# Optimization experiments

Hardware: AMD Instinct MI355X
Metric: run time of the kernel (lower is better)

Reference implementation:

```python
import jax, jax.numpy as jnp
import numpy as np

N, E, F, R, L, B = 50000, 800000, 64, 20, 2, 64
RC = 5.0
ZMAX = 100
LN2 = 0.6931471805599453

def ssp(x):
    # shifted softplus: softplus(x) - log(2)
    return jax.nn.softplus(x) - LN2

def setup_inputs() -> dict:
    key = jax.random.key(0)
    ks = jax.random.split(key, 32)
    w = lambda i, shape: jax.random.normal(ks[i], shape, dtype=jnp.float32) * 0.05
    inp = {
        'z': jax.random.randint(ks[0], (N,), 0, ZMAX + 1),
        'pos': jax.random.normal(ks[1], (N, 3), dtype=jnp.float32) * 3.0,
        'edge_index': jax.random.randint(ks[2], (2, E), 0, N),
        'batch_idx': jnp.sort(jax.random.randint(ks[3], (N,), 0, B)),
        'emb': jax.random.normal(ks[4], (ZMAX + 1, F), dtype=jnp.float32),
        'phi_W': w(5, (L, 3 * F, F)), 'phi_b': w(6, (L, 3 * F)),
        'filt_W1': w(7, (L, F, R)), 'filt_b1': w(8, (L, F)),
        'filt_W2': w(9, (L, 3 * F, F)), 'filt_b2': w(10, (L, 3 * F)),
        'U_W': w(11, (L, F, F)), 'V_W': w(12, (L, F, F)),
        'a_W1': w(13, (L, F, 2 * F)), 'a_b1': w(14, (L, F)),
        'a_W2': w(15, (L, 3 * F, F)), 'a_b2': w(16, (L, 3 * F)),
        'e_W1': w(17, (F // 2, F)), 'e_b1': w(18, (F // 2,)),
        'e_W2': w(19, (1, F // 2)), 'e_b2': w(20, (1,)),
        'dip_w': w(21, (F,)),
    }
    return inp

def reference(z, pos, edge_index, batch_idx, emb, phi_W, phi_b,
              filt_W1, filt_b1, filt_W2, filt_b2, U_W, V_W,
              a_W1, a_b1, a_W2, a_b2, e_W1, e_b1, e_W2, e_b2, dip_w):
    src, dst = edge_index[0], edge_index[1]
    s = emb[z]                               # (N, F)
    v = jnp.zeros((N, F, 3), dtype=s.dtype)  # (N, F, 3)

    # edge geometry
    r_vec = pos[dst] - pos[src]              # (E, 3)
    r_norm = jnp.linalg.norm(r_vec, axis=-1)
    r_hat = r_vec / jnp.maximum(r_norm, 1e-8)[:, None]
    # Gaussian RBF on [0, RC], widths = grid spacing
    mu = jnp.linspace(0.0, RC, R, dtype=s.dtype)
    width = mu[1] - mu[0]
    e_ij = jnp.exp(-((r_norm[:, None] - mu[None, :]) ** 2) / (2.0 * width * width))
    fc = 0.5 * (jnp.cos(jnp.pi * r_norm / RC) + 1.0) * (r_norm < RC)
    e_ij = e_ij * fc[:, None]                # (E, R)

    for l in range(L):
        # message block
        filt = ssp(e_ij @ filt_W1[l].T + filt_b1[l]) @ filt_W2[l].T + filt_b2[l]  # (E, 3F)
        W_s, W_v, W_r = jnp.split(filt, 3, axis=-1)
        phi = s[dst] @ phi_W[l].T + phi_b[l]                                       # (E, 3F)
        phi_s, phi_v, phi_r = jnp.split(phi, 3, axis=-1)
        m_s = W_s * phi_s                                                          # (E, F)
        m_v = W_v[:, :, None] * v[dst] + (W_r * phi_r)[:, :, None] * r_hat[:, None, :]  # (E, F, 3)
        s = s + jax.ops.segment_sum(m_s, src, num_segments=N)
        v = v + jax.ops.segment_sum(m_v, src, num_segments=N)
        # update block
        Uv = jnp.einsum('nfd,gf->ngd', v, U_W[l])
        Vv = jnp.einsum('nfd,gf->ngd', v, V_W[l])
        Vv_norm_sq = jnp.sum(Vv * Vv, axis=-1)                                     # (N, F)
        a = ssp(jnp.concatenate([s, Vv_norm_sq], axis=-1) @ a_W1[l].T + a_b1[l]) @ a_W2[l].T + a_b2[l]
        a_ss, a_sv, a_vv = jnp.split(a, 3, axis=-1)
        inner = jnp.sum(Uv * Vv, axis=-1)
        s = s + a_ss + a_sv * inner
        v = v + a_vv[:, :, None] * Uv

    # heads
    eps_i = (ssp(s @ e_W1.T + e_b1) @ e_W2.T + e_b2)[:, 0]  # (N,)
    energy = jax.ops.segment_sum(eps_i, batch_idx, num_segments=B)
    mu_i = jnp.sum(v * dip_w[None, :, None], axis=1)         # (N, 3)
    mu_mol = jax.ops.segment_sum(mu_i, batch_idx, num_segments=B)
    dipole = jnp.linalg.norm(mu_mol, axis=-1)
    charges = jnp.zeros((N,), dtype=s.dtype)
    return energy, dipole, charges
```

## Files before the change

### kernel.cpp

```cpp
#include <hip/hip_runtime.h>
#include <math.h>

static constexpr int N  = 50000;
static constexpr int E  = 800000;
static constexpr int F  = 64;
static constexpr int R  = 20;
static constexpr int NL = 2;
static constexpr int B  = 64;
static constexpr float RC   = 5.0f;
static constexpr float LN2F = 0.6931471805599453f;
static constexpr float WIDTH  = RC / (R - 1);
static constexpr float INV2W2 = 1.0f / (2.0f * WIDTH * WIDTH);
static constexpr float PI_F = 3.14159265358979323846f;

static constexpr int   NB     = 4096;
static constexpr float DR     = RC / NB;
static constexpr float INV_DR = NB / RC;
static constexpr int   IZERO  = NB + 1;
static constexpr int   TENTA  = NB + 2;

static constexpr int NBLK_SCAN = (N + 255) / 256;

typedef __attribute__((ext_vector_type(8))) short bf16x8;
typedef __attribute__((ext_vector_type(4))) float f32x4;
typedef __attribute__((ext_vector_type(3))) unsigned uint32x3;

__device__ __forceinline__ float ssp_f(float x) {
    return fmaxf(x, 0.0f) + log1pf(__expf(-fabsf(x))) - LN2F;
}

__device__ __forceinline__ short f2bf(float x) {
    unsigned u = __builtin_bit_cast(unsigned, x);
    unsigned r = (u + 0x7fffu + ((u >> 16) & 1u)) >> 16;
    return (short)r;
}
__device__ __forceinline__ float bf_lo(unsigned u) {
    return __builtin_bit_cast(float, u << 16);
}
__device__ __forceinline__ float bf_hi(unsigned u) {
    return __builtin_bit_cast(float, u & 0xffff0000u);
}

__global__ void k_hist(const int* __restrict__ ei, int* __restrict__ cnt) {
    int e = blockIdx.x * blockDim.x + threadIdx.x;
    if (e < E) atomicAdd(&cnt[ei[e]], 1);
}

__global__ void k_scan_a(const int* __restrict__ cnt, int* __restrict__ bsum) {
    __shared__ int part[256];
    const int t = threadIdx.x;
    const int idx = blockIdx.x * 256 + t;
    int v = (idx < N) ? ((cnt[idx] + 1) & ~1) : 0;
    part[t] = v;
    __syncthreads();
    for (int d = 1; d < 256; d <<= 1) {
        int x = (t >= d) ? part[t - d] : 0;
        __syncthreads();
        part[t] += x;
        __syncthreads();
    }
    if (t == 255) bsum[blockIdx.x] = part[255];
}

__global__ void k_scan_b(const int* __restrict__ bsum, int* __restrict__ bpre,
                         int* __restrict__ offN) {
    __shared__ int part[256];
    const int t = threadIdx.x;
    int v = (t < NBLK_SCAN) ? bsum[t] : 0;
    part[t] = v;
    __syncthreads();
    for (int d = 1; d < 256; d <<= 1) {
        int x = (t >= d) ? part[t - d] : 0;
        __syncthreads();
        part[t] += x;
        __syncthreads();
    }
    if (t < NBLK_SCAN) bpre[t] = part[t] - v;
    if (t == NBLK_SCAN - 1) *offN = part[t];
}

__global__ void k_scan_c(const int* __restrict__ cnt, const int* __restrict__ bpre,
                         int* __restrict__ off, int* __restrict__ cur,
                         uint4* __restrict__ edata) {
    __shared__ int part[256];
    const int t = threadIdx.x;
    const int idx = blockIdx.x * 256 + t;
    int vraw = (idx < N) ? cnt[idx] : 0;
    int v = (vraw + 1) & ~1;
    part[t] = v;
    __syncthreads();
    for (int d = 1; d < 256; d <<= 1) {
        int x = (t >= d) ? part[t - d] : 0;
        __syncthreads();
        part[t] += x;
        __syncthreads();
    }
    if (idx < N) {
        int e = bpre[blockIdx.x] + part[t] - v;
        off[idx] = e;
        cur[idx] = e;
        if (vraw & 1) {
            uint4 nil;
            nil.x = (unsigned)idx * 256u;
            nil.y = (unsigned)IZERO * 512u;
            nil.z = 0u; nil.w = 0u;
            edata[e + vraw] = nil;
        }
    }
}

__global__ void k_scatter(const int* __restrict__ ei, int* __restrict__ cur,
                          const float* __restrict__ pos, uint4* __restrict__ edata) {
    int e = blockIdx.x * blockDim.x + threadIdx.x;
    if (e >= E) return;
    int src = ei[e], dst = ei[E + e];
    int p = atomicAdd(&cur[src], 1);
    float qx = pos[dst * 3 + 0] - pos[src * 3 + 0];
    float qy = pos[dst * 3 + 1] - pos[src * 3 + 1];
    float qz = pos[dst * 3 + 2] - pos[src * 3 + 2];
    float rn = sqrtf(qx * qx + qy * qy + qz * qz);
    float invn = 1.0f / fmaxf(rn, 1e-8f);
    int i = (int)(rn * INV_DR + 0.5f);
    if (i > NB) i = NB;
    uint4 rec;
    rec.x = (unsigned)dst * 256u;
    rec.y = (unsigned)i * 512u;
    rec.z = (unsigned)(unsigned short)f2bf(qx * invn)
          | ((unsigned)(unsigned short)f2bf(qy * invn) << 16);
    rec.w = (unsigned)(unsigned short)f2bf(qz * invn);
    edata[p] = rec;
}

__global__ void k_table(const float* __restrict__ fW1, const float* __restrict__ fb1,
                        const float* __restrict__ fW2, const float* __restrict__ fb2,
                        unsigned short* __restrict__ Tp) {
    __shared__ float sh[4][F];
    const int wid  = threadIdx.x >> 6;
    const int lane = threadIdx.x & 63;
    const int gid  = blockIdx.x * 4 + wid;
    if (gid >= NL * (NB + 1)) return;
    const int l   = gid / (NB + 1);
    const int row = gid % (NB + 1);
    const float r = (float)row * DR;
    const float fc = (r < RC) ? 0.5f * (__cosf(PI_F * r * (1.0f / RC)) + 1.0f) : 0.0f;

    float acc = fb1[l * F + lane];
    const float* w1 = fW1 + (size_t)l * F * R + (size_t)lane * R;
    #pragma unroll
    for (int rr = 0; rr < R; rr++) {
        float dmu = r - rr * WIDTH;
        float er = __expf(-dmu * dmu * INV2W2) * fc;
        acc = fmaf(er, w1[rr], acc);
    }
    sh[wid][lane] = ssp_f(acc);
    __syncthreads();
    unsigned short* TpL = Tp + (size_t)l * TENTA * 256;
    #pragma unroll
    for (int p = 0; p < 3; p++) {
        int c = p * 64 + lane;
        float a = fb2[l * 192 + c];
        const float* w2 = fW2 + ((size_t)l * 192 + c) * 64;
        #pragma unroll 8
        for (int k = 0; k < F; k++) a = fmaf(sh[wid][k], w2[k], a);
        TpL[(size_t)row * 256 + lane * 4 + p] = (unsigned short)f2bf(a);
    }
    TpL[(size_t)row * 256 + lane * 4 + 3] = 0;
    if (row == 0) {
        #pragma unroll
        for (int j = 0; j < 4; j++)
            TpL[(size_t)IZERO * 256 + lane * 4 + j] = 0;
    }
}

__launch_bounds__(256)
__global__ void k_pack0(float* __restrict__ s, const int* __restrict__ z,
                        const float* __restrict__ emb,
                        const float* __restrict__ PW, const float* __restrict__ Pb,
                        unsigned* __restrict__ ndA0) {
    __shared__ float sbuf[4][F];
    const int lane = threadIdx.x & 63;
    const int wid  = threadIdx.x >> 6;
    const int gwave = blockIdx.x * 4 + wid;
    const int nwaves = gridDim.x * 4;

    float wsr[F], wrr[F];
    {
        const float* rs = PW + (size_t)lane * 64;
        const float* rr = PW + (size_t)(128 + lane) * 64;
        #pragma unroll
        for (int k = 0; k < F; k += 4) {
            float4 a = *(const float4*)(rs + k);
            wsr[k] = a.x; wsr[k+1] = a.y; wsr[k+2] = a.z; wsr[k+3] = a.w;
            float4 b = *(const float4*)(rr + k);
            wrr[k] = b.x; wrr[k+1] = b.y; wrr[k+2] = b.z; wrr[k+3] = b.w;
        }
    }
    const float bs = Pb[lane], br = Pb[128 + lane];

    for (int n = gwave; n < N; n += nwaves) {
        float sv = emb[(size_t)z[n] * F + lane];
        s[(size_t)n * F + lane] = sv;
        sbuf[wid][lane] = sv;
        float as = bs, ar = br;
        #pragma unroll
        for (int k = 0; k < F; k += 4) {
            float4 s4 = *(const float4*)&sbuf[wid][k];
            as = fmaf(s4.x, wsr[k],   as); as = fmaf(s4.y, wsr[k+1], as);
            as = fmaf(s4.z, wsr[k+2], as); as = fmaf(s4.w, wsr[k+3], as);
            ar = fmaf(s4.x, wrr[k],   ar); ar = fmaf(s4.y, wrr[k+1], ar);
            ar = fmaf(s4.z, wrr[k+2], ar); ar = fmaf(s4.w, wrr[k+3], ar);
        }
        ndA0[(size_t)n * 64 + lane] = (unsigned)(unsigned short)f2bf(as)
                                    | ((unsigned)(unsigned short)f2bf(ar) << 16);
    }
}

template<bool ACCUMV>
__device__ __forceinline__ void consume_edge(const uint4 ed, const uint2 t,
                                             const uint32x3 r,
                                             float& ms, float& mv0, float& mv1, float& mv2) {
    const float Ws = bf_lo(t.x);
    const float Wr = bf_lo(t.y);
    ms = fmaf(Ws, bf_lo(r.x), ms);
    const float c = Wr * bf_hi(r.x);
    const float rhx = bf_lo(ed.z), rhy = bf_hi(ed.z), rhz = bf_lo(ed.w);
    if (ACCUMV) {
        const float Wv = bf_hi(t.x);
        mv0 = fmaf(Wv, bf_lo(r.y), fmaf(c, rhx, mv0));
        mv1 = fmaf(Wv, bf_hi(r.y), fmaf(c, rhy, mv1));
        mv2 = fmaf(Wv, bf_lo(r.z), fmaf(c, rhz, mv2));
    } else {
        mv0 = fmaf(c, rhx, mv0);
        mv1 = fmaf(c, rhy, mv1);
        mv2 = fmaf(c, rhz, mv2);
    }
}

template<bool ACCUMV>
__device__ __forceinline__ uint2 load_tbl(const char* __restrict__ tb, unsigned yoff) {
    return *(const uint2*)(tb + yoff);
}
template<bool ACCUMV>
__device__ __forceinline__ uint32x3 load_rec(const char* __restrict__ rb0,
                                             const char* __restrict__ rbV, unsigned xoff) {
    uint32x3 r;
    if (ACCUMV) {
        r = *(const uint32x3*)(rbV + (size_t)xoff * 3);
    } else {
        r.x = *(const unsigned*)(rb0 + xoff); r.y = 0; r.z = 0;
    }
    return r;
}

template<bool ACCUMV>
__launch_bounds__(128, 8)
__global__ void k_gather(const uint4* __restrict__ edata, const int* __restrict__ off,
                         const unsigned short* __restrict__ TpL,
                         const unsigned* __restrict__ ndA0,
                         const unsigned* __restrict__ ndAV,
                         float* __restrict__ s, float* __restrict__ v) {
    const int lane = threadIdx.x & 63;
    const int wv   = threadIdx.x >> 6;
    const int n = blockIdx.x * 2 + wv;
    if (n >= N) return;
    const int base = off[n], end = off[n + 1];

    const char* tb  = (const char*)TpL  + lane * 8;
    const char* rb0 = (const char*)ndA0 + lane * 4;
    const char* rbV = (const char*)ndAV + lane * 12;

    float ms = 0.f, mv0 = 0.f, mv1 = 0.f, mv2 = 0.f;

    if (base < end) {
        uint4 ed0 = edata[base];
        uint4 ed1 = edata[base + 1];
        uint2    t0 = load_tbl<ACCUMV>(tb, ed0.y);
        uint32x3 r0 = load_rec<ACCUMV>(rb0, rbV, ed0.x);

        for (int k = base; k < end - 2; ++k) {
            uint4 ed2 = edata[k + 2];
            uint2    t1 = load_tbl<ACCUMV>(tb, ed1.y);
            uint32x3 r1 = load_rec<ACCUMV>(rb0, rbV, ed1.x);
            consume_edge<ACCUMV>(ed0, t0, r0, ms, mv0, mv1, mv2);
            ed0 = ed1; t0 = t1; r0 = r1;
            ed1 = ed2;
        }
        uint2    t1 = load_tbl<ACCUMV>(tb, ed1.y);
        uint32x3 r1 = load_rec<ACCUMV>(rb0, rbV, ed1.x);
        consume_edge<ACCUMV>(ed0, t0, r0, ms, mv0, mv1, mv2);
        consume_edge<ACCUMV>(ed1, t1, r1, ms, mv0, mv1, mv2);
    }

    s[(size_t)n * F + lane] += ms;
    float* vo = v + (size_t)n * 3 * F + lane;
    if (ACCUMV) {
        vo[0]     += mv0;
        vo[F]     += mv1;
        vo[2 * F] += mv2;
    } else {
        vo[0] = mv0; vo[F] = mv1; vo[2 * F] = mv2;
    }
}

__device__ __forceinline__ bf16x8 load_wfrag(const float* __restrict__ Wp, int ldk,
                                             int nrow, int k0) {
    const float* p = Wp + (size_t)nrow * ldk + k0;
    float4 a = *(const float4*)p;
    float4 b = *(const float4*)(p + 4);
    bf16x8 r;
    r[0] = f2bf(a.x); r[1] = f2bf(a.y); r[2] = f2bf(a.z); r[3] = f2bf(a.w);
    r[4] = f2bf(b.x); r[5] = f2bf(b.y); r[6] = f2bf(b.z); r[7] = f2bf(b.w);
    return r;
}

template<bool DO_PACK>
__launch_bounds__(256)
__global__ void k_update_mfma(float* __restrict__ s, float* __restrict__ v,
                              const float* __restrict__ U_W, const float* __restrict__ V_W,
                              const float* __restrict__ aW1, const float* __restrict__ ab1,
                              const float* __restrict__ aW2, const float* __restrict__ ab2,
                              const float* __restrict__ PW, const float* __restrict__ Pb,
                              unsigned* __restrict__ ndAV) {
    __shared__ short vlds[96 * 72];
    __shared__ short xlds[32 * 136];
    __shared__ short hlds[32 * 72];

    const int tid = threadIdx.x;
    const int l   = tid & 63;
    const int w   = tid >> 6;
    const int lo  = l & 15;
    const int hi  = l >> 4;

    bf16x8 ufr[2], vfr[2], w1fr[4], w2fr[3][2];
    #pragma unroll
    for (int kk = 0; kk < 2; kk++) {
        ufr[kk] = load_wfrag(U_W, 64, w * 16 + lo, kk * 32 + hi * 8);
        vfr[kk] = load_wfrag(V_W, 64, w * 16 + lo, kk * 32 + hi * 8);
    }
    #pragma unroll
    for (int kk = 0; kk < 4; kk++)
        w1fr[kk] = load_wfrag(aW1, 128, w * 16 + lo, kk * 32 + hi * 8);
    #pragma unroll
    for (int p = 0; p < 3; p++)
        #pragma unroll
        for (int kk = 0; kk < 2; kk++)
            w2fr[p][kk] = load_wfrag(aW2, 64, p * 64 + w * 16 + lo, kk * 32 + hi * 8);

    bf16x8 pws[2], pwr[2];
    float pbs = 0.f, pbr = 0.f;
    if (DO_PACK) {
        #pragma unroll
        for (int kk = 0; kk < 2; kk++) {
            pws[kk] = load_wfrag(PW, 64, w * 16 + lo, kk * 32 + hi * 8);
            pwr[kk] = load_wfrag(PW, 64, 128 + w * 16 + lo, kk * 32 + hi * 8);
        }
        pbs = Pb[w * 16 + lo];
        pbr = Pb[128 + w * 16 + lo];
    }

    const float ab1c  = ab1[w * 16 + lo];
    const float ab2c0 = ab2[w * 16 + lo];
    const float ab2c1 = ab2[64 + w * 16 + lo];
    const float ab2c2 = ab2[128 + w * 16 + lo];
    const int g = w * 16 + lo;

    for (int half = 0; half < 2; half++) {
        const int n0 = blockIdx.x * 64 + half * 32;
        if (half) __syncthreads();

        for (int u = tid; u < 96 * 8; u += 256) {
            int row = u >> 3, oct = u & 7;
            int d = row >> 5, nn = row & 31;
            int n = min(n0 + nn, N - 1);
            const float* src = v + ((size_t)n * 3 + d) * 64 + oct * 8;
            float4 a = *(const float4*)src;
            float4 b = *(const float4*)(src + 4);
            bf16x8 t;
            t[0] = f2bf(a.x); t[1] = f2bf(a.y); t[2] = f2bf(a.z); t[3] = f2bf(a.w);
            t[4] = f2bf(b.x); t[5] = f2bf(b.y); t[6] = f2bf(b.z); t[7] = f2bf(b.w);
            *(bf16x8*)&vlds[row * 72 + oct * 8] = t;
        }
        for (int u = tid; u < 32 * 8; u += 256) {
            int nn = u >> 3, oct = u & 7;
            int n = min(n0 + nn, N - 1);
            const float* src = s + (size_t)n * 64 + oct * 8;
            float4 a = *(const float4*)src;
            float4 b = *(const float4*)(src + 4);
            bf16x8 t;
            t[0] = f2bf(a.x); t[1] = f2bf(a.y); t[2] = f2bf(a.z); t[3] = f2bf(a.w);
            t[4] = f2bf(b.x); t[5] = f2bf(b.y); t[6] = f2bf(b.z); t[7] = f2bf(b.w);
            *(bf16x8*)&xlds[nn * 136 + oct * 8] = t;
        }
        __syncthreads();

        f32x4 cu[6], cv[6];
        #pragma unroll
        for (int mt = 0; mt < 6; mt++) { cu[mt] = (f32x4)0.0f; cv[mt] = (f32x4)0.0f; }
        #pragma unroll
        for (int kk = 0; kk < 2; kk++) {
            #pragma unroll
            for (int mt = 0; mt < 6; mt++) {
                bf16x8 af = *(const bf16x8*)&vlds[(mt * 16 + lo) * 72 + kk * 32 + hi * 8];
                cu[mt] = __builtin_amdgcn_mfma_f32_16x16x32_bf16(af, ufr[kk], cu[mt], 0, 0, 0);
                cv[mt] = __builtin_amdgcn_mfma_f32_16x16x32_bf16(af, vfr[kk], cv[mt], 0, 0, 0);
            }
        }

        f32x4 inn[2];
        #pragma unroll
        for (int nt = 0; nt < 2; nt++) {
            #pragma unroll
            for (int r = 0; r < 4; r++) {
                float vs = 0.f, ii = 0.f;
                #pragma unroll
                for (int d = 0; d < 3; d++) {
                    float a = cu[d * 2 + nt][r], b = cv[d * 2 + nt][r];
                    vs = fmaf(b, b, vs);
                    ii = fmaf(a, b, ii);
                }
                inn[nt][r] = ii;
                int nl = nt * 16 + hi * 4 + r;
                xlds[nl * 136 + 64 + w * 16 + lo] = f2bf(vs);
            }
        }
        __syncthreads();

        f32x4 c2[2];
        c2[0] = (f32x4)0.0f; c2[1] = (f32x4)0.0f;
        #pragma unroll
        for (int kk = 0; kk < 4; kk++) {
            #pragma unroll
            for (int mt = 0; mt < 2; mt++) {
                bf16x8 af = *(const bf16x8*)&xlds[(mt * 16 + lo) * 136 + kk * 32 + hi * 8];
                c2[mt] = __builtin_amdgcn_mfma_f32_16x16x32_bf16(af, w1fr[kk], c2[mt], 0, 0, 0);
            }
        }
        #pragma unroll
        for (int mt = 0; mt < 2; mt++)
            #pragma unroll
            for (int r = 0; r < 4; r++) {
                float hv = ssp_f(c2[mt][r] + ab1c);
                hlds[(mt * 16 + hi * 4 + r) * 72 + w * 16 + lo] = f2bf(hv);
            }
        __syncthreads();

        f32x4 c3[2][3];
        #pragma unroll
        for (int mt = 0; mt < 2; mt++)
            #pragma unroll
            for (int p = 0; p < 3; p++) c3[mt][p] = (f32x4)0.0f;
        #pragma unroll
        for (int kk = 0; kk < 2; kk++) {
            #pragma unroll
            for (int mt = 0; mt < 2; mt++) {
                bf16x8 af = *(const bf16x8*)&hlds[(mt * 16 + lo) * 72 + kk * 32 + hi * 8];
                #pragma unroll
                for (int p = 0; p < 3; p++)
                    c3[mt][p] = __builtin_amdgcn_mfma_f32_16x16x32_bf16(af, w2fr[p][kk], c3[mt][p], 0, 0, 0);
            }
        }

        float snew[2][4];
        #pragma unroll
        for (int mt = 0; mt < 2; mt++) {
            #pragma unroll
            for (int r = 0; r < 4; r++) {
                int n = n0 + mt * 16 + hi * 4 + r;
                if (n >= N) { snew[mt][r] = 0.f; continue; }
                float a_ss = c3[mt][0][r] + ab2c0;
                float a_sv = c3[mt][1][r] + ab2c1;
                float a_vv = c3[mt][2][r] + ab2c2;
                size_t si = (size_t)n * 64 + g;
                float sn = s[si] + a_ss + a_sv * inn[mt][r];
                s[si] = sn;
                snew[mt][r] = sn;
                float vn[3];
                #pragma unroll
                for (int d = 0; d < 3; d++) {
                    size_t vi = ((size_t)n * 3 + d) * 64 + g;
                    vn[d] = v[vi] + a_vv * cu[d * 2 + mt][r];
                    v[vi] = vn[d];
                }
                if (DO_PACK) {
                    unsigned* pp = ndAV + ((size_t)n * 64 + g) * 3;
                    pp[1] = (unsigned)(unsigned short)f2bf(vn[0])
                          | ((unsigned)(unsigned short)f2bf(vn[1]) << 16);
                    pp[2] = (unsigned)(unsigned short)f2bf(vn[2]);
                }
            }
        }

        if (DO_PACK) {
            __syncthreads();
            #pragma unroll
            for (int mt = 0; mt < 2; mt++)
                #pragma unroll
                for (int r = 0; r < 4; r++)
                    hlds[(mt * 16 + hi * 4 + r) * 72 + g] = f2bf(snew[mt][r]);
            __syncthreads();

            f32x4 cs[2], cr[2];
            cs[0] = (f32x4)0.0f; cs[1] = (f32x4)0.0f;
            cr[0] = (f32x4)0.0f; cr[1] = (f32x4)0.0f;
            #pragma unroll
            for (int kk = 0; kk < 2; kk++) {
                #pragma unroll
                for (int mt = 0; mt < 2; mt++) {
                    bf16x8 af = *(const bf16x8*)&hlds[(mt * 16 + lo) * 72 + kk * 32 + hi * 8];
                    cs[mt] = __builtin_amdgcn_mfma_f32_16x16x32_bf16(af, pws[kk], cs[mt], 0, 0, 0);
                    cr[mt] = __builtin_amdgcn_mfma_f32_16x16x32_bf16(af, pwr[kk], cr[mt], 0, 0, 0);
                }
            }
            #pragma unroll
            for (int mt = 0; mt < 2; mt++) {
                #pragma unroll
                for (int r = 0; r < 4; r++) {
                    int n = n0 + mt * 16 + hi * 4 + r;
                    if (n >= N) continue;
                    ndAV[((size_t)n * 64 + g) * 3] =
                          (unsigned)(unsigned short)f2bf(cs[mt][r] + pbs)
                        | ((unsigned)(unsigned short)f2bf(cr[mt][r] + pbr) << 16);
                }
            }
        }
    }
}

__global__ void k_heads(const float* __restrict__ s, const float* __restrict__ v,
                        const int* __restrict__ batch_idx,
                        const float* __restrict__ eW1, const float* __restrict__ eb1,
                        const float* __restrict__ eW2, const float* __restrict__ eb2,
                        const float* __restrict__ dip_w,
                        float* __restrict__ eacc, float* __restrict__ macc) {
    __shared__ float se[B];
    __shared__ float sm[3][B];
    if (threadIdx.x < B) se[threadIdx.x] = 0.0f;
    if (threadIdx.x < 3 * B) sm[threadIdx.x >> 6][threadIdx.x & 63] = 0.0f;
    __syncthreads();
    int n = blockIdx.x * blockDim.x + threadIdx.x;
    if (n < N) {
        int b = batch_idx[n];
        float sr[F];
        #pragma unroll
        for (int f = 0; f < F; f += 4) {
            float4 t = *(const float4*)&s[(size_t)n * F + f];
            sr[f] = t.x; sr[f+1] = t.y; sr[f+2] = t.z; sr[f+3] = t.w;
        }
        float eps = eb2[0];
        for (int jj = 0; jj < F / 2; jj++) {
            float acc = eb1[jj];
            #pragma unroll
            for (int f = 0; f < F; f++)
                acc = fmaf(sr[f], eW1[jj * F + f], acc);
            eps = fmaf(eW2[jj], ssp_f(acc), eps);
        }
        atomicAdd(&se[b], eps);
        #pragma unroll
        for (int d = 0; d < 3; d++) {
            float m = 0.0f;
            #pragma unroll 8
            for (int f = 0; f < F; f++)
                m = fmaf(v[((size_t)n * 3 + d) * F + f], dip_w[f], m);
            atomicAdd(&sm[d][b], m);
        }
    }
    __syncthreads();
    if (threadIdx.x < B) atomicAdd(&eacc[threadIdx.x], se[threadIdx.x]);
    if (threadIdx.x >= B && threadIdx.x < 4 * B) {
        int d = (threadIdx.x >> 6) - 1, b = threadIdx.x & 63;
        atomicAdd(&macc[d * B + b], sm[d][b]);
    }
}

__global__ void k_final(const float* __restrict__ eacc, const float* __restrict__ macc,
                        float* __restrict__ out) {
    int b = threadIdx.x;
    if (b < B) {
        out[b] = eacc[b];
        float mx = macc[b], my = macc[B + b], mz = macc[2 * B + b];
        out[B + b] = sqrtf(mx * mx + my * my + mz * mz);
    }
}

extern "C" void kernel_launch(void* const* d_in, const int* in_sizes, int n_in,
                              void* d_out, int out_size, void* d_ws, size_t ws_size,
                              hipStream_t stream) {
    const int*   z     = (const int*)d_in[0];
    const float* pos   = (const float*)d_in[1];
    const int*   ei    = (const int*)d_in[2];
    const int*   bidx  = (const int*)d_in[3];
    const float* emb   = (const float*)d_in[4];
    const float* phi_W = (const float*)d_in[5];
    const float* phi_b = (const float*)d_in[6];
    const float* fW1   = (const float*)d_in[7];
    const float* fb1   = (const float*)d_in[8];
    const float* fW2   = (const float*)d_in[9];
    const float* fb2   = (const float*)d_in[10];
    const float* U_W   = (const float*)d_in[11];
    const float* V_W   = (const float*)d_in[12];
    const float* aW1   = (const float*)d_in[13];
    const float* ab1   = (const float*)d_in[14];
    const float* aW2   = (const float*)d_in[15];
    const float* ab2   = (const float*)d_in[16];
    const float* eW1   = (const float*)d_in[17];
    const float* eb1   = (const float*)d_in[18];
    const float* eW2   = (const float*)d_in[19];
    const float* eb2   = (const float*)d_in[20];
    const float* dip_w = (const float*)d_in[21];
    float* out = (float*)d_out;

    float* ws = (float*)d_ws;
    float* s    = ws;
    float* v    = s + (size_t)N * F;
    unsigned* ndA0 = (unsigned*)(v + (size_t)N * F * 3);
    unsigned* ndAV = ndA0 + (size_t)N * 64;
    unsigned short* Tp = (unsigned short*)(ndAV + (size_t)N * 64 * 3);
    float* eacc = (float*)(Tp + (size_t)NL * TENTA * 256);
    float* macc = eacc + B;
    int*   cnt  = (int*)(macc + 3 * B);
    int*   off  = cnt  + N;
    int*   cur  = off  + N + 1;
    int*   bsum = cur  + N;
    int*   bpre = bsum + 256;
    uint4* edata = (uint4*)(((uintptr_t)(bpre + 256) + 15) & ~(uintptr_t)15);

    hipMemsetAsync(cnt,  0, sizeof(int) * N, stream);
    hipMemsetAsync(eacc, 0, sizeof(float) * 4 * B, stream);
    hipMemsetAsync(out + 2 * B, 0, sizeof(float) * (size_t)N, stream);

    k_hist<<<(E + 255) / 256, 256, 0, stream>>>(ei, cnt);
    k_scan_a<<<NBLK_SCAN, 256, 0, stream>>>(cnt, bsum);
    k_scan_b<<<1, 256, 0, stream>>>(bsum, bpre, off + N);
    k_scan_c<<<NBLK_SCAN, 256, 0, stream>>>(cnt, bpre, off, cur, edata);
    k_scatter<<<(E + 255) / 256, 256, 0, stream>>>(ei, cur, pos, edata);
    k_table<<<(NL * (NB + 1) + 3) / 4, 256, 0, stream>>>(fW1, fb1, fW2, fb2, Tp);

    const int gblocks = (N + 1) / 2;
    const int ublocks = (N + 63) / 64;
    k_pack0<<<512, 256, 0, stream>>>(s, z, emb, phi_W, phi_b, ndA0);
    k_gather<false><<<gblocks, 128, 0, stream>>>(edata, off, Tp, ndA0, ndAV, s, v);
    k_update_mfma<true><<<ublocks, 256, 0, stream>>>(s, v,
        U_W, V_W, aW1, ab1, aW2, ab2,
        phi_W + (size_t)192 * 64, phi_b + 192, ndAV);
    k_gather<true><<<gblocks, 128, 0, stream>>>(edata, off,
        Tp + (size_t)TENTA * 256, ndA0, ndAV, s, v);
    k_update_mfma<false><<<ublocks, 256, 0, stream>>>(s, v,
        U_W + 4096, V_W + 4096, aW1 + 8192, ab1 + F, aW2 + 12288, ab2 + 192,
        nullptr, nullptr, nullptr);

    k_heads<<<(N + 255) / 256, 256, 0, stream>>>(s, v, bidx, eW1, eb1, eW2, eb2,
                                                 dip_w, eacc, macc);
    k_final<<<1, 64, 0, stream>>>(eacc, macc, out);
}
```

Baseline: 487.4 us.

## Fuse final update block with energy and dipole heads into one MFMA kernel

The last layer's update kernel now computes the energy head via MFMA and the dipole projection via wave shuffles, instead of writing s and v back and launching a separate scalar heads kernel. This removes a full read of s and v and one launch, and skips the final s/v stores. The energy head runs in bf16 on MFMA, which reduces precision. Per-node global atomics replace block-level shared reductions, which adds atomic contention on the per-molecule accumulators.

Result: slower. 799.7 us (+64.1%).

```diff
diff --git a/kernel.cpp b/kernel.cpp
--- a/kernel.cpp
+++ b/kernel.cpp
@@ -313,7 +313,6 @@
     return r;
 }
 
-template<bool DO_PACK>
 __launch_bounds__(256)
 __global__ void k_update_mfma(float* __restrict__ s, float* __restrict__ v,
                               const float* __restrict__ U_W, const float* __restrict__ V_W,
@@ -347,16 +346,13 @@
             w2fr[p][kk] = load_wfrag(aW2, 64, p * 64 + w * 16 + lo, kk * 32 + hi * 8);
 
     bf16x8 pws[2], pwr[2];
-    float pbs = 0.f, pbr = 0.f;
-    if (DO_PACK) {
-        #pragma unroll
-        for (int kk = 0; kk < 2; kk++) {
-            pws[kk] = load_wfrag(PW, 64, w * 16 + lo, kk * 32 + hi * 8);
-            pwr[kk] = load_wfrag(PW, 64, 128 + w * 16 + lo, kk * 32 + hi * 8);
-        }
-        pbs = Pb[w * 16 + lo];
-        pbr = Pb[128 + w * 16 + lo];
-    }
+    #pragma unroll
+    for (int kk = 0; kk < 2; kk++) {
+        pws[kk] = load_wfrag(PW, 64, w * 16 + lo, kk * 32 + hi * 8);
+        pwr[kk] = load_wfrag(PW, 64, 128 + w * 16 + lo, kk * 32 + hi * 8);
+    }
+    const float pbs = Pb[w * 16 + lo];
+    const float pbr = Pb[128 + w * 16 + lo];
 
     const float ab1c  = ab1[w * 16 + lo];
     const float ab2c0 = ab2[w * 16 + lo];
@@ -481,94 +477,278 @@
                     vn[d] = v[vi] + a_vv * cu[d * 2 + mt][r];
                     v[vi] = vn[d];
                 }
-                if (DO_PACK) {
-                    unsigned* pp = ndAV + ((size_t)n * 64 + g) * 3;
-                    pp[1] = (unsigned)(unsigned short)f2bf(vn[0])
-                          | ((unsigned)(unsigned short)f2bf(vn[1]) << 16);
-                    pp[2] = (unsigned)(unsigned short)f2bf(vn[2]);
+                unsigned* pp = ndAV + ((size_t)n * 64 + g) * 3;
+                pp[1] = (unsigned)(unsigned short)f2bf(vn[0])
+                      | ((unsigned)(unsigned short)f2bf(vn[1]) << 16);
+                pp[2] = (unsigned)(unsigned short)f2bf(vn[2]);
+            }
+        }
+
+        __syncthreads();
+        #pragma unroll
+        for (int mt = 0; mt < 2; mt++)
+            #pragma unroll
+            for (int r = 0; r < 4; r++)
+                hlds[(mt * 16 + hi * 4 + r) * 72 + g] = f2bf(snew[mt][r]);
+        __syncthreads();
+
+        f32x4 cs[2], cr[2];
+        cs[0] = (f32x4)0.0f; cs[1] = (f32x4)0.0f;
+        cr[0] = (f32x4)0.0f; cr[1] = (f32x4)0.0f;
+        #pragma unroll
+        for (int kk = 0; kk < 2; kk++) {
+            #pragma unroll
+            for (int mt = 0; mt < 2; mt++) {
+                bf16x8 af = *(const bf16x8*)&hlds[(mt * 16 + lo) * 72 + kk * 32 + hi * 8];
+                cs[mt] = __builtin_amdgcn_mfma_f32_16x16x32_bf16(af, pws[kk], cs[mt], 0, 0, 0);
+                cr[mt] = __builtin_amdgcn_mfma_f32_16x16x32_bf16(af, pwr[kk], cr[mt], 0, 0, 0);
+            }
+        }
+        #pragma unroll
+        for (int mt = 0; mt < 2; mt++) {
+            #pragma unroll
+            for (int r = 0; r < 4; r++) {
+                int n = n0 + mt * 16 + hi * 4 + r;
+                if (n >= N) continue;
+                ndAV[((size_t)n * 64 + g) * 3] =
+                      (unsigned)(unsigned short)f2bf(cs[mt][r] + pbs)
+                    | ((unsigned)(unsigned short)f2bf(cr[mt][r] + pbr) << 16);
+            }
+        }
+    }
+}
+
+__launch_bounds__(256)
+__global__ void k_update_heads(const float* __restrict__ s, const float* __restrict__ v,
+                               const float* __restrict__ U_W, const float* __restrict__ V_W,
+                               const float* __restrict__ aW1, const float* __restrict__ ab1,
+                               const float* __restrict__ aW2, const float* __restrict__ ab2,
+                               const float* __restrict__ eW1, const float* __restrict__ eb1,
+                               const float* __restrict__ eW2, const float* __restrict__ eb2,
+                               const float* __restrict__ dip_w,
+                               const int* __restrict__ bidx,
+                               float* __restrict__ eacc, float* __restrict__ macc) {
+    __shared__ short vlds[96 * 72];
+    __shared__ short xlds[32 * 136];
+    __shared__ short hlds[32 * 72];
+    __shared__ float epsb[2][2][16];
+    __shared__ float dmub[4][2][16][3];
+
+    const int tid = threadIdx.x;
+    const int l   = tid & 63;
+    const int w   = tid >> 6;
+    const int lo  = l & 15;
+    const int hi  = l >> 4;
+
+    bf16x8 ufr[2], vfr[2], w1fr[4], w2fr[3][2], e1fr[2];
+    #pragma unroll
+    for (int kk = 0; kk < 2; kk++) {
+        ufr[kk] = load_wfrag(U_W, 64, w * 16 + lo, kk * 32 + hi * 8);
+        vfr[kk] = load_wfrag(V_W, 64, w * 16 + lo, kk * 32 + hi * 8);
+        e1fr[kk] = load_wfrag(eW1, 64, (w & 1) * 16 + lo, kk * 32 + hi * 8);
+    }
+    #pragma unroll
+    for (int kk = 0; kk < 4; kk++)
+        w1fr[kk] = load_wfrag(aW1, 128, w * 16 + lo, kk * 32 + hi * 8);
+    #pragma unroll
+    for (int p = 0; p < 3; p++)
+        #pragma unroll
+        for (int kk = 0; kk < 2; kk++)
+            w2fr[p][kk] = load_wfrag(aW2, 64, p * 64 + w * 16 + lo, kk * 32 + hi * 8);
+
+    const float ab1c  = ab1[w * 16 + lo];
+    const float ab2c0 = ab2[w * 16 + lo];
+    const float ab2c1 = ab2[64 + w * 16 + lo];
+    const float ab2c2 = ab2[128 + w * 16 + lo];
+    const float eb1v  = eb1[(w & 1) * 16 + lo];
+    const float ew2v  = eW2[(w & 1) * 16 + lo];
+    const float eb2c  = eb2[0];
+    const int g = w * 16 + lo;
+    const float dwv = dip_w[g];
+
+    for (int half = 0; half < 2; half++) {
+        const int n0 = blockIdx.x * 64 + half * 32;
+        if (half) __syncthreads();
+
+        for (int u = tid; u < 96 * 8; u += 256) {
+            int row = u >> 3, oct = u & 7;
+            int d = row >> 5, nn = row & 31;
+            int n = min(n0 + nn, N - 1);
+            const float* src = v + ((size_t)n * 3 + d) * 64 + oct * 8;
+            float4 a = *(const float4*)src;
+            float4 b = *(const float4*)(src + 4);
+            bf16x8 t;
+            t[0] = f2bf(a.x); t[1] = f2bf(a.y); t[2] = f2bf(a.z); t[3] = f2bf(a.w);
+            t[4] = f2bf(b.x); t[5] = f2bf(b.y); t[6] = f2bf(b.z); t[7] = f2bf(b.w);
+            *(bf16x8*)&vlds[row * 72 + oct * 8] = t;
+        }
+        for (int u = tid; u < 32 * 8; u += 256) {
+            int nn = u >> 3, oct = u & 7;
+            int n = min(n0 + nn, N - 1);
+            const float* src = s + (size_t)n * 64 + oct * 8;
+            float4 a = *(const float4*)src;
+            float4 b = *(const float4*)(src + 4);
+            bf16x8 t;
+            t[0] = f2bf(a.x); t[1] = f2bf(a.y); t[2] = f2bf(a.z); t[3] = f2bf(a.w);
+            t[4] = f2bf(b.x); t[5] = f2bf(b.y); t[6] = f2bf(b.z); t[7] = f2bf(b.w);
+            *(bf16x8*)&xlds[nn * 136 + oct * 8] = t;
+        }
+        __syncthreads();
+
+        f32x4 cu[6], cv[6];
+        #pragma unroll
+        for (int mt = 0; mt < 6; mt++) { cu[mt] = (f32x4)0.0f; cv[mt] = (f32x4)0.0f; }
+        #pragma unroll
+        for (int kk = 0; kk < 2; kk++) {
+            #pragma unroll
+            for (int mt = 0; mt < 6; mt++) {
+                bf16x8 af = *(const bf16x8*)&vlds[(mt * 16 + lo) * 72 + kk * 32 + hi * 8];
+                cu[mt] = __builtin_amdgcn_mfma_f32_16x16x32_bf16(af, ufr[kk], cu[mt], 0, 0, 0);
+                cv[mt] = __builtin_amdgcn_mfma_f32_16x16x32_bf16(af, vfr[kk], cv[mt], 0, 0, 0);
+            }
+        }
+
+        f32x4 inn[2];
+        #pragma unroll
+        for (int nt = 0; nt < 2; nt++) {
+            #pragma unroll
+            for (int r = 0; r < 4; r++) {
+                float vs = 0.f, ii = 0.f;
+                #pragma unroll
+                for (int d = 0; d < 3; d++) {
+                    float a = cu[d * 2 + nt][r], b = cv[d * 2 + nt][r];
+                    vs = fmaf(b, b, vs);
+                    ii = fmaf(a, b, ii);
                 }
-            }
-        }
-
-        if (DO_PACK) {
-            __syncthreads();
-            #pragma unroll
-            for (int mt = 0; mt < 2; mt++)
+                inn[nt][r] = ii;
+                int nl = nt * 16 + hi * 4 + r;
+                xlds[nl * 136 + 64 + w * 16 + lo] = f2bf(vs);
+            }
+        }
+        __syncthreads();
+
+        f32x4 c2[2];
+        c2[0] = (f32x4)0.0f; c2[1] = (f32x4)0.0f;
+        #pragma unroll
+        for (int kk = 0; kk < 4; kk++) {
+            #pragma unroll
+            for (int mt = 0; mt < 2; mt++) {
+                bf16x8 af = *(const bf16x8*)&xlds[(mt * 16 + lo) * 136 + kk * 32 + hi * 8];
+                c2[mt] = __builtin_amdgcn_mfma_f32_16x16x32_bf16(af, w1fr[kk], c2[mt], 0, 0, 0);
+            }
+        }
+        #pragma unroll
+        for (int mt = 0; mt < 2; mt++)
+            #pragma unroll
+            for (int r = 0; r < 4; r++) {
+                float hv = ssp_f(c2[mt][r] + ab1c);
+                hlds[(mt * 16 + hi * 4 + r) * 72 + w * 16 + lo] = f2bf(hv);
+            }
+        __syncthreads();
+
+        f32x4 c3[2][3];
+        #pragma unroll
+        for (int mt = 0; mt < 2; mt++)
+            #pragma unroll
+            for (int p = 0; p < 3; p++) c3[mt][p] = (f32x4)0.0f;
+        #pragma unroll
+        for (int kk = 0; kk < 2; kk++) {
+            #pragma unroll
+            for (int mt = 0; mt < 2; mt++) {
+                bf16x8 af = *(const bf16x8*)&hlds[(mt * 16 + lo) * 72 + kk * 32 + hi * 8];
+                #pragma unroll
+                for (int p = 0; p < 3; p++)
+                    c3[mt][p] = __builtin_amdgcn_mfma_f32_16x16x32_bf16(af, w2fr[p][kk], c3[mt][p], 0, 0, 0);
+            }
+        }
+
+        float snew[2][4];
+        float vnk[2][4][3];
+        #pragma unroll
+        for (int mt = 0; mt < 2; mt++) {
+            #pragma unroll
+            for (int r = 0; r < 4; r++) {
+                int n = n0 + mt * 16 + hi * 4 + r;
+                if (n >= N) {
+                    snew[mt][r] = 0.f;
+                    vnk[mt][r][0] = vnk[mt][r][1] = vnk[mt][r][2] = 0.f;
+                    continue;
+                }
+                float a_ss = c3[mt][0][r] + ab2c0;
+                float a_sv = c3[mt][1][r] + ab2c1;
+                float a_vv = c3[mt][2][r] + ab2c2;
+                size_t si = (size_t)n * 64 + g;
+                snew[mt][r] = s[si] + a_ss + a_sv * inn[mt][r];
+                #pragma unroll
+                for (int d = 0; d < 3; d++) {
+                    size_t vi = ((size_t)n * 3 + d) * 64 + g;
+                    vnk[mt][r][d] = v[vi] + a_vv * cu[d * 2 + mt][r];
+                }
+            }
+        }
+
+        __syncthreads();
+        #pragma unroll
+        for (int mt = 0; mt < 2; mt++)
+            #pragma unroll
+            for (int r = 0; r < 4; r++)
+                hlds[(mt * 16 + hi * 4 + r) * 72 + g] = f2bf(snew[mt][r]);
+        __syncthreads();
+
+        {
+            const int a2 = w >> 1;
+            f32x4 cx = (f32x4)0.0f;
+            #pragma unroll
+            for (int kk = 0; kk < 2; kk++) {
+                bf16x8 af = *(const bf16x8*)&hlds[(a2 * 16 + lo) * 72 + kk * 32 + hi * 8];
+                cx = __builtin_amdgcn_mfma_f32_16x16x32_bf16(af, e1fr[kk], cx, 0, 0, 0);
+            }
+            float part[4];
+            #pragma unroll
+            for (int r = 0; r < 4; r++)
+                part[r] = ssp_f(cx[r] + eb1v) * ew2v;
+            #pragma unroll
+            for (int m2 = 1; m2 < 16; m2 <<= 1)
                 #pragma unroll
                 for (int r = 0; r < 4; r++)
-                    hlds[(mt * 16 + hi * 4 + r) * 72 + g] = f2bf(snew[mt][r]);
-            __syncthreads();
-
-            f32x4 cs[2], cr[2];
-            cs[0] = (f32x4)0.0f; cs[1] = (f32x4)0.0f;
-            cr[0] = (f32x4)0.0f; cr[1] = (f32x4)0.0f;
-            #pragma unroll
-            for (int kk = 0; kk < 2; kk++) {
+                    part[r] += __shfl_xor(part[r], m2);
+            if (lo == 0)
                 #pragma unroll
-                for (int mt = 0; mt < 2; mt++) {
-                    bf16x8 af = *(const bf16x8*)&hlds[(mt * 16 + lo) * 72 + kk * 32 + hi * 8];
-                    cs[mt] = __builtin_amdgcn_mfma_f32_16x16x32_bf16(af, pws[kk], cs[mt], 0, 0, 0);
-                    cr[mt] = __builtin_amdgcn_mfma_f32_16x16x32_bf16(af, pwr[kk], cr[mt], 0, 0, 0);
+                for (int r = 0; r < 4; r++)
+                    epsb[a2][w & 1][hi * 4 + r] = part[r];
+        }
+
+        #pragma unroll
+        for (int mt = 0; mt < 2; mt++)
+            #pragma unroll
+            for (int r = 0; r < 4; r++)
+                #pragma unroll
+                for (int d = 0; d < 3; d++) {
+                    float val = dwv * vnk[mt][r][d];
+                    #pragma unroll
+                    for (int m2 = 1; m2 < 16; m2 <<= 1)
+                        val += __shfl_xor(val, m2);
+                    if (lo == 0) dmub[w][mt][hi * 4 + r][d] = val;
                 }
-            }
-            #pragma unroll
-            for (int mt = 0; mt < 2; mt++) {
-                #pragma unroll
-                for (int r = 0; r < 4; r++) {
-                    int n = n0 + mt * 16 + hi * 4 + r;
-                    if (n >= N) continue;
-                    ndAV[((size_t)n * 64 + g) * 3] =
-                          (unsigned)(unsigned short)f2bf(cs[mt][r] + pbs)
-                        | ((unsigned)(unsigned short)f2bf(cr[mt][r] + pbr) << 16);
-                }
-            }
-        }
-    }
-}
-
-__global__ void k_heads(const float* __restrict__ s, const float* __restrict__ v,
-                        const int* __restrict__ batch_idx,
-                        const float* __restrict__ eW1, const float* __restrict__ eb1,
-                        const float* __restrict__ eW2, const float* __restrict__ eb2,
-                        const float* __restrict__ dip_w,
-                        float* __restrict__ eacc, float* __restrict__ macc) {
-    __shared__ float se[B];
-    __shared__ float sm[3][B];
-    if (threadIdx.x < B) se[threadIdx.x] = 0.0f;
-    if (threadIdx.x < 3 * B) sm[threadIdx.x >> 6][threadIdx.x & 63] = 0.0f;
-    __syncthreads();
-    int n = blockIdx.x * blockDim.x + threadIdx.x;
-    if (n < N) {
-        int b = batch_idx[n];
-        float sr[F];
-        #pragma unroll
-        for (int f = 0; f < F; f += 4) {
-            float4 t = *(const float4*)&s[(size_t)n * F + f];
-            sr[f] = t.x; sr[f+1] = t.y; sr[f+2] = t.z; sr[f+3] = t.w;
-        }
-        float eps = eb2[0];
-        for (int jj = 0; jj < F / 2; jj++) {
-            float acc = eb1[jj];
-            #pragma unroll
-            for (int f = 0; f < F; f++)
-                acc = fmaf(sr[f], eW1[jj * F + f], acc);
-            eps = fmaf(eW2[jj], ssp_f(acc), eps);
-        }
-        atomicAdd(&se[b], eps);
-        #pragma unroll
-        for (int d = 0; d < 3; d++) {
-            float m = 0.0f;
-            #pragma unroll 8
-            for (int f = 0; f < F; f++)
-                m = fmaf(v[((size_t)n * 3 + d) * F + f], dip_w[f], m);
-            atomicAdd(&sm[d][b], m);
-        }
-    }
-    __syncthreads();
-    if (threadIdx.x < B) atomicAdd(&eacc[threadIdx.x], se[threadIdx.x]);
-    if (threadIdx.x >= B && threadIdx.x < 4 * B) {
-        int d = (threadIdx.x >> 6) - 1, b = threadIdx.x & 63;
-        atomicAdd(&macc[d * B + b], sm[d][b]);
+        __syncthreads();
+
+        if (tid < 32) {
+            int nn = tid, a2 = nn >> 4, idx = nn & 15;
+            int n = n0 + nn;
+            if (n < N) {
+                float ev = epsb[a2][0][idx] + epsb[a2][1][idx] + eb2c;
+                atomicAdd(&eacc[bidx[n]], ev);
+            }
+        } else if (tid >= 64 && tid < 160) {
+            int t2 = tid - 64;
+            int nn = t2 / 3, d = t2 % 3;
+            int n = n0 + nn;
+            if (n < N) {
+                float mv = dmub[0][nn >> 4][nn & 15][d] + dmub[1][nn >> 4][nn & 15][d]
+                         + dmub[2][nn >> 4][nn & 15][d] + dmub[3][nn >> 4][nn & 15][d];
+                atomicAdd(&macc[d * B + bidx[n]], mv);
+            }
+        }
     }
 }
 
@@ -639,16 +819,14 @@
     const int ublocks = (N + 63) / 64;
     k_pack0<<<512, 256, 0, stream>>>(s, z, emb, phi_W, phi_b, ndA0);
     k_gather<false><<<gblocks, 128, 0, stream>>>(edata, off, Tp, ndA0, ndAV, s, v);
-    k_update_mfma<true><<<ublocks, 256, 0, stream>>>(s, v,
+    k_update_mfma<<<ublocks, 256, 0, stream>>>(s, v,
         U_W, V_W, aW1, ab1, aW2, ab2,
         phi_W + (size_t)192 * 64, phi_b + 192, ndAV);
     k_gather<true><<<gblocks, 128, 0, stream>>>(edata, off,
         Tp + (size_t)TENTA * 256, ndA0, ndAV, s, v);
-    k_update_mfma<false><<<ublocks, 256, 0, stream>>>(s, v,
+    k_update_heads<<<ublocks, 256, 0, stream>>>(s, v,
         U_W + 4096, V_W + 4096, aW1 + 8192, ab1 + F, aW2 + 12288, ab2 + 192,
-        nullptr, nullptr, nullptr);
-
-    k_heads<<<(N + 255) / 256, 256, 0, stream>>>(s, v, bidx, eW1, eb1, eW2, eb2,
-                                                 dip_w, eacc, macc);
+        eW1, eb1, eW2, eb2, dip_w, bidx, eacc, macc);
+
     k_final<<<1, 64, 0, stream>>>(eacc, macc, out);
 }
```
